# Kernel optimization log

Measured on AMD Instinct MI355X. Metric: run time of the kernel, lower is better.

## Reference

```python
import jax, jax.numpy as jnp
import numpy as np

N = 50000   # num_embs = num nodes
E = 800000  # num edges
D = 256     # feature dim
L = 4       # num layers
EPS = 1e-5


def setup_inputs() -> dict:
    key = jax.random.key(0)
    ks = jax.random.split(key, 8)
    scale = 1.0 / np.sqrt(D)
    return {
        "x": jax.random.normal(ks[0], (N, D), dtype=jnp.float32),  # ignored by forward
        "edge_index": jax.random.randint(ks[1], (2, E), 0, N, dtype=jnp.int32),
        "edge_weight": jax.random.uniform(ks[2], (E,), dtype=jnp.float32),
        "emb_weight": jax.random.normal(ks[3], (N, D), dtype=jnp.float32),
        "ln_w": jnp.ones((L, D), dtype=jnp.float32),
        "ln_b": jnp.zeros((L, D), dtype=jnp.float32),
        "conv_w": jax.random.normal(ks[4], (L, D, D), dtype=jnp.float32) * scale,
        "conv_b": jnp.zeros((L, D), dtype=jnp.float32),
        "post_w": jax.random.normal(ks[5], (D, D), dtype=jnp.float32) * scale,
        "post_b": jnp.zeros((D,), dtype=jnp.float32),
    }


def _layer_norm(h, w, b):
    mu = jnp.mean(h, axis=-1, keepdims=True)
    var = jnp.mean(jnp.square(h - mu), axis=-1, keepdims=True)
    return (h - mu) * jax.lax.rsqrt(var + EPS) * w + b


def reference(x, edge_index, edge_weight, emb_weight, ln_w, ln_b, conv_w, conv_b, post_w, post_b):
    # GCNConv semantics (PyG defaults): add self-loops (weight 1), symmetric norm.
    loop = jnp.arange(N, dtype=edge_index.dtype)
    src = jnp.concatenate([edge_index[0], loop])
    dst = jnp.concatenate([edge_index[1], loop])
    w = jnp.concatenate([edge_weight, jnp.ones((N,), edge_weight.dtype)])
    deg = jax.ops.segment_sum(w, dst, num_segments=N)
    dinv = jnp.where(deg > 0, jax.lax.rsqrt(jnp.maximum(deg, 1e-12)), 0.0)
    coef = (dinv[src] * w * dinv[dst])[:, None]  # [E+N, 1]

    h = emb_weight  # forward ignores x; cond_emb is None
    for i in range(L):
        z = _layer_norm(h, ln_w[i], ln_b[i])          # node LayerNorm
        zw = z @ conv_w[i]                             # linear transform
        agg = jax.ops.segment_sum(coef * zw[src], dst, num_segments=N)
        z = agg + conv_b[i]
        z = jax.nn.gelu(z, approximate=False)          # torch GELU is exact
        h = z + h                                      # residual (dropout=0)
    return h @ post_w + post_b
```

## Files before the change

### kernel.cpp

```cpp
#include <hip/hip_runtime.h>
#include <hip/hip_bf16.h>

#define N_NODES 50000
#define N_EDGES 800000
#define DIM     256
#define NLAYERS 4
#define EPS     1e-5f
#define SCAN_B  196
#define MASK40  ((1ULL << 40) - 1)
#define EPACK_CAP (N_EDGES + 15 * N_NODES + 32)
#define STRIDE  260
#define KSTRIDE (N_NODES * 32)

typedef __bf16 bf16x8 __attribute__((ext_vector_type(8)));
typedef float  f32x4  __attribute__((ext_vector_type(4)));
typedef float  f32x2  __attribute__((ext_vector_type(2)));
typedef unsigned short u16x8 __attribute__((ext_vector_type(8)));
typedef unsigned short u16x4 __attribute__((ext_vector_type(4)));
typedef int            i32x4 __attribute__((ext_vector_type(4)));
typedef unsigned int   u32x2 __attribute__((ext_vector_type(2)));

__device__ __forceinline__ unsigned short f2b(float f) {
    __hip_bfloat16 h = __float2bfloat16(f);
    return __builtin_bit_cast(unsigned short, h);
}
__device__ __forceinline__ float b2f(unsigned short u) {
    unsigned int v = ((unsigned int)u) << 16;
    return __builtin_bit_cast(float, v);
}
__device__ __forceinline__ float gelu_exact(float x) {
    float ax = fabsf(x) * 0.70710678118654752f;
    float t  = 1.0f / (1.0f + 0.3275911f * ax);
    float p  = t * (0.254829592f + t * (-0.284496736f +
               t * (1.421413741f + t * (-1.453152027f + t * 1.061405429f))));
    float er = 1.0f - p * __expf(-ax * ax);
    er = (x < 0.0f) ? -er : er;
    return 0.5f * x * (1.0f + er);
}
__device__ __forceinline__ unsigned int pack_fp8x4(float a, float b, float c, float d) {
    int v = 0;
    v = __builtin_amdgcn_cvt_pk_fp8_f32(a, b, v, false);
    v = __builtin_amdgcn_cvt_pk_fp8_f32(c, d, v, true);
    return (unsigned int)v;
}

__global__ __launch_bounds__(256) void hist_kernel(const int* __restrict__ dst,
                                                   const float* __restrict__ w,
                                                   unsigned long long* __restrict__ cnt64,
                                                   int* __restrict__ rank) {
    int e = blockIdx.x * 256 + threadIdx.x;
    if (e >= N_EDGES) return;
    int d = dst[e];
    unsigned long long wfix = (unsigned long long)(w[e] * 4294967296.0f);
    unsigned long long old = atomicAdd(&cnt64[d], (1ULL << 40) | wfix);
    rank[e] = (int)(old >> 40);
}

__global__ __launch_bounds__(256) void scan_a_kernel(const unsigned long long* __restrict__ cnt64,
                                                     float* __restrict__ dinv,
                                                     int* __restrict__ bsum) {
    __shared__ int l[256];
    int i = blockIdx.x * 256 + threadIdx.x;
    int pc = 0;
    if (i < N_NODES) {
        unsigned long long v = cnt64[i];
        int cnt = (int)(v >> 40);
        float sw = (float)(v & MASK40) * 2.3283064365386963e-10f;
        dinv[i] = rsqrtf(1.0f + sw);
        pc = (cnt + 15) & ~15;
    }
    l[threadIdx.x] = pc;
    __syncthreads();
    for (int o = 128; o > 0; o >>= 1) {
        if (threadIdx.x < o) l[threadIdx.x] += l[threadIdx.x + o];
        __syncthreads();
    }
    if (threadIdx.x == 0) bsum[blockIdx.x] = l[0];
}

__global__ __launch_bounds__(256) void scan_b_kernel(const int* __restrict__ bsum,
                                                     int* __restrict__ boff,
                                                     int* __restrict__ rowptr) {
    __shared__ int l[256];
    int t = threadIdx.x;
    l[t] = (t < SCAN_B) ? bsum[t] : 0;
    __syncthreads();
    if (t == 0) {
        int run = 0;
        for (int j = 0; j < SCAN_B; ++j) { int v = l[j]; l[j] = run; run += v; }
        rowptr[N_NODES] = run;
    }
    __syncthreads();
    boff[t] = l[t];
}

__global__ __launch_bounds__(256) void scan_c_kernel(const unsigned long long* __restrict__ cnt64,
                                                     const int* __restrict__ boff,
                                                     int* __restrict__ rowptr) {
    __shared__ int l[256];
    int i = blockIdx.x * 256 + threadIdx.x;
    int pc = 0;
    if (i < N_NODES) {
        int cnt = (int)(cnt64[i] >> 40);
        pc = (cnt + 15) & ~15;
    }
    l[threadIdx.x] = pc;
    __syncthreads();
    if (threadIdx.x == 0) {
        int run = 0;
        for (int j = 0; j < 256; ++j) { int v = l[j]; l[j] = run; run += v; }
    }
    __syncthreads();
    if (i < N_NODES) rowptr[i] = boff[blockIdx.x] + l[threadIdx.x];
}

__global__ __launch_bounds__(256) void fill_kernel(const int* __restrict__ src,
                                                   const int* __restrict__ dst,
                                                   const float* __restrict__ w,
                                                   const float* __restrict__ dinv,
                                                   const int* __restrict__ rowptr,
                                                   const int* __restrict__ rank,
                                                   int2* __restrict__ epack) {
    int e = blockIdx.x * 256 + threadIdx.x;
    if (e >= N_EDGES) return;
    int s = src[e], d = dst[e];
    float c = dinv[s] * w[e] * dinv[d];
    int p = rowptr[d] + rank[e];
    epack[p] = make_int2(s << 8, __float_as_int(c));
}

__global__ __launch_bounds__(256) void convw_kernel(const float* __restrict__ conv_w,
                                                    const float* __restrict__ post_w,
                                                    unsigned short* __restrict__ Wt) {
    int idx = blockIdx.x * 256 + threadIdx.x;
    if (idx >= 5 * 65536) return;
    int m  = idx >> 16;
    int r  = idx & 65535;
    int ks = r >> 13;
    int n  = (r >> 5) & 255;
    int ke = r & 31;
    int k  = ks * 32 + ke;
    float v = (m < 4) ? conv_w[m * 65536 + k * 256 + n] : post_w[k * 256 + n];
    Wt[idx] = f2b(v);
}

__global__ __launch_bounds__(256) void ln_cast_kernel(const float* __restrict__ H,
                                                      const float* __restrict__ lnw,
                                                      const float* __restrict__ lnb,
                                                      unsigned char* __restrict__ Z8,
                                                      unsigned short* __restrict__ Hbf) {
    int row = blockIdx.x * 4 + (threadIdx.x >> 6);
    int lane = threadIdx.x & 63;
    const float4 x = *(const float4*)(H + (size_t)row * DIM + lane * 4);
    float s = x.x + x.y + x.z + x.w;
    for (int o = 32; o > 0; o >>= 1) s += __shfl_xor(s, o);
    float mu = s * (1.0f / DIM);
    float d0 = x.x - mu, d1 = x.y - mu, d2 = x.z - mu, d3 = x.w - mu;
    float v = d0 * d0 + d1 * d1 + d2 * d2 + d3 * d3;
    for (int o = 32; o > 0; o >>= 1) v += __shfl_xor(v, o);
    float rs = rsqrtf(v * (1.0f / DIM) + EPS);
    const float4 ww = *(const float4*)(lnw + lane * 4);
    const float4 bb = *(const float4*)(lnb + lane * 4);
    float z0 = d0 * rs * ww.x + bb.x;
    float z1 = d1 * rs * ww.y + bb.y;
    float z2 = d2 * rs * ww.z + bb.z;
    float z3 = d3 * rs * ww.w + bb.w;
    *(unsigned int*)(Z8 + (size_t)row * DIM + lane * 4) = pack_fp8x4(z0, z1, z2, z3);
    ushort4 h4;
    h4.x = f2b(x.x); h4.y = f2b(x.y); h4.z = f2b(x.z); h4.w = f2b(x.w);
    *(ushort4*)(Hbf + (size_t)row * DIM + lane * 4) = h4;
}

__global__ __launch_bounds__(256) void agg_kernel(const unsigned char* __restrict__ Z8,
                                                  const int* __restrict__ rowptr,
                                                  const int2* __restrict__ epack,
                                                  const float* __restrict__ dinv,
                                                  unsigned short* __restrict__ AGG) {
    int node = blockIdx.x * 4 + (threadIdx.x >> 6);
    int lane = threadIdx.x & 63;
    int g = lane >> 5;
    int colB = (lane & 31) * 8;

    float di = dinv[node];
    float scg = (g == 0) ? di * di : 0.0f;
    const u32x2 zs = *(const u32x2*)(Z8 + (size_t)node * DIM + colB);
    f32x2 a0, a1, a2, a3;
    {
        f32x2 p0 = __builtin_amdgcn_cvt_pk_f32_fp8(zs[0], false);
        f32x2 p1 = __builtin_amdgcn_cvt_pk_f32_fp8(zs[0], true);
        f32x2 p2 = __builtin_amdgcn_cvt_pk_f32_fp8(zs[1], false);
        f32x2 p3 = __builtin_amdgcn_cvt_pk_f32_fp8(zs[1], true);
        a0 = scg * p0; a1 = scg * p1; a2 = scg * p2; a3 = scg * p3;
    }

    int e0 = rowptr[node], e1 = rowptr[node + 1];
    for (int e = e0; e < e1; e += 16) {
        const int2* pp = epack + e + 8 * g;
        const i32x4 q0 = *(const i32x4*)pp;
        const i32x4 q1 = *(const i32x4*)(pp + 2);
        const i32x4 q2 = *(const i32x4*)(pp + 4);
        const i32x4 q3 = *(const i32x4*)(pp + 6);
        const u32x2 v0 = *(const u32x2*)(Z8 + q0[0] + colB);
        const u32x2 v1 = *(const u32x2*)(Z8 + q0[2] + colB);
        const u32x2 v2 = *(const u32x2*)(Z8 + q1[0] + colB);
        const u32x2 v3 = *(const u32x2*)(Z8 + q1[2] + colB);
        const u32x2 v4 = *(const u32x2*)(Z8 + q2[0] + colB);
        const u32x2 v5 = *(const u32x2*)(Z8 + q2[2] + colB);
        const u32x2 v6 = *(const u32x2*)(Z8 + q3[0] + colB);
        const u32x2 v7 = *(const u32x2*)(Z8 + q3[2] + colB);
        float c0 = __int_as_float(q0[1]), c1 = __int_as_float(q0[3]);
        float c2 = __int_as_float(q1[1]), c3 = __int_as_float(q1[3]);
        float c4 = __int_as_float(q2[1]), c5 = __int_as_float(q2[3]);
        float c6 = __int_as_float(q3[1]), c7 = __int_as_float(q3[3]);
        #pragma unroll
        for (int h = 0; h < 8; ++h) {
            u32x2 vv; float cc;
            switch (h) {
                case 0: vv = v0; cc = c0; break;
                case 1: vv = v1; cc = c1; break;
                case 2: vv = v2; cc = c2; break;
                case 3: vv = v3; cc = c3; break;
                case 4: vv = v4; cc = c4; break;
                case 5: vv = v5; cc = c5; break;
                case 6: vv = v6; cc = c6; break;
                default: vv = v7; cc = c7; break;
            }
            f32x2 p0 = __builtin_amdgcn_cvt_pk_f32_fp8(vv[0], false);
            f32x2 p1 = __builtin_amdgcn_cvt_pk_f32_fp8(vv[0], true);
            f32x2 p2 = __builtin_amdgcn_cvt_pk_f32_fp8(vv[1], false);
            f32x2 p3 = __builtin_amdgcn_cvt_pk_f32_fp8(vv[1], true);
            a0 += cc * p0; a1 += cc * p1; a2 += cc * p2; a3 += cc * p3;
        }
    }
    float a[8] = {a0[0], a0[1], a1[0], a1[1], a2[0], a2[1], a3[0], a3[1]};
    #pragma unroll
    for (int j = 0; j < 8; ++j) a[j] += __shfl_xor(a[j], 32);

    if (g == 0) {
        u16x8 z;
        #pragma unroll
        for (int j = 0; j < 8; ++j) z[j] = f2b(a[j]);
        int ks  = colB >> 5;
        int off = colB & 31;
        *(u16x8*)(AGG + (size_t)ks * KSTRIDE + node * 32 + off) = z;
    }
}

__global__ __launch_bounds__(256, 4) void gemm_fused_kernel(const unsigned short* __restrict__ A,
                                                            const unsigned short* __restrict__ Bt,
                                                            const float* __restrict__ bias,
                                                            unsigned short* __restrict__ Hbf,
                                                            const float* __restrict__ lnw,
                                                            const float* __restrict__ lnb,
                                                            unsigned char* __restrict__ Z8,
                                                            int doLN) {
    __shared__ unsigned short stile[32 * STRIDE];
    int tid = threadIdx.x;
    int wave = tid >> 6;
    int lane = tid & 63;
    int q = lane >> 4;
    int c16 = lane & 15;
    int mbase = blockIdx.x * 32;
    int cbase = wave * 64;

    int aoff[2];
    #pragma unroll
    for (int nt = 0; nt < 2; ++nt) {
        int row = mbase + nt * 16 + c16;
        if (row >= N_NODES) row = N_NODES - 1;
        aoff[nt] = row * 32 + q * 8;
    }
    int woff[4];
    #pragma unroll
    for (int ct = 0; ct < 4; ++ct)
        woff[ct] = (cbase + ct * 16 + c16) * 32 + q * 8;

    f32x4 acc[2][4] = {};
    #pragma unroll
    for (int ks = 0; ks < 8; ++ks) {
        bf16x8 nf[2], wf[4];
        #pragma unroll
        for (int nt = 0; nt < 2; ++nt)
            nf[nt] = __builtin_bit_cast(bf16x8, *(const u16x8*)(A + (size_t)ks * KSTRIDE + aoff[nt]));
        #pragma unroll
        for (int ct = 0; ct < 4; ++ct)
            wf[ct] = __builtin_bit_cast(bf16x8, *(const u16x8*)(Bt + ks * 8192 + woff[ct]));
        #pragma unroll
        for (int nt = 0; nt < 2; ++nt)
            #pragma unroll
            for (int ct = 0; ct < 4; ++ct)
                acc[nt][ct] = __builtin_amdgcn_mfma_f32_16x16x32_bf16(wf[ct], nf[nt], acc[nt][ct], 0, 0, 0);
    }

    #pragma unroll
    for (int nt = 0; nt < 2; ++nt) {
        int row = nt * 16 + c16;
        #pragma unroll
        for (int ct = 0; ct < 4; ++ct) {
            int col = cbase + ct * 16 + q * 4;
            u16x4 pk;
            pk[0] = f2b(acc[nt][ct][0]);
            pk[1] = f2b(acc[nt][ct][1]);
            pk[2] = f2b(acc[nt][ct][2]);
            pk[3] = f2b(acc[nt][ct][3]);
            *(u16x4*)&stile[row * STRIDE + col] = pk;
        }
    }
    __syncthreads();

    int r  = tid >> 3;
    int cb = (tid & 7) * 32;
    int node = mbase + r;
    if (node < N_NODES) {
        float h[32];
        float psum = 0.0f, psq = 0.0f;
        #pragma unroll
        for (int i = 0; i < 4; ++i) {
            const u16x8 sv = *(const u16x8*)&stile[r * STRIDE + cb + i * 8];
            const f32x4 b0 = *(const f32x4*)(bias + cb + i * 8);
            const f32x4 b1 = *(const f32x4*)(bias + cb + i * 8 + 4);
            const u16x8 hv = *(const u16x8*)(Hbf + (size_t)node * DIM + cb + i * 8);
            #pragma unroll
            for (int j = 0; j < 8; ++j) {
                float v = b2f(sv[j]) + (j < 4 ? b0[j] : b1[j - 4]);
                float hn = gelu_exact(v) + b2f(hv[j]);
                h[i * 8 + j] = hn;
                psum += hn;
                psq += hn * hn;
            }
        }
        #pragma unroll
        for (int i = 0; i < 4; ++i) {
            u16x8 hw;
            #pragma unroll
            for (int j = 0; j < 8; ++j) hw[j] = f2b(h[i * 8 + j]);
            *(u16x8*)(Hbf + (size_t)node * DIM + cb + i * 8) = hw;
        }
        if (doLN) {
            psum += __shfl_xor(psum, 1);
            psum += __shfl_xor(psum, 2);
            psum += __shfl_xor(psum, 4);
            psq  += __shfl_xor(psq, 1);
            psq  += __shfl_xor(psq, 2);
            psq  += __shfl_xor(psq, 4);
            float mu = psum * (1.0f / DIM);
            float var = fmaxf(psq * (1.0f / DIM) - mu * mu, 0.0f);
            float rs = rsqrtf(var + EPS);
            #pragma unroll
            for (int i2 = 0; i2 < 2; ++i2) {
                int c0 = cb + i2 * 16;
                unsigned int pk[4];
                #pragma unroll
                for (int k = 0; k < 4; ++k) {
                    const f32x4 ww = *(const f32x4*)(lnw + c0 + k * 4);
                    const f32x4 lb = *(const f32x4*)(lnb + c0 + k * 4);
                    int hb = i2 * 16 + k * 4;
                    float y0 = (h[hb + 0] - mu) * rs * ww[0] + lb[0];
                    float y1 = (h[hb + 1] - mu) * rs * ww[1] + lb[1];
                    float y2 = (h[hb + 2] - mu) * rs * ww[2] + lb[2];
                    float y3 = (h[hb + 3] - mu) * rs * ww[3] + lb[3];
                    pk[k] = pack_fp8x4(y0, y1, y2, y3);
                }
                uint4 st = make_uint4(pk[0], pk[1], pk[2], pk[3]);
                *(uint4*)(Z8 + (size_t)node * DIM + c0) = st;
            }
        }
    }
}

__global__ __launch_bounds__(256, 4) void gemm_out_kernel(const unsigned short* __restrict__ A,
                                                          const unsigned short* __restrict__ Bt,
                                                          float* __restrict__ C,
                                                          const float* __restrict__ bias) {
    int tid = threadIdx.x;
    int wave = tid >> 6;
    int lane = tid & 63;
    int q = lane >> 4;
    int c16 = lane & 15;
    int mbase = blockIdx.x * 32;
    int cbase = wave * 64;

    const unsigned short* aptr[2];
    #pragma unroll
    for (int nt = 0; nt < 2; ++nt) {
        int row = mbase + nt * 16 + c16;
        if (row >= N_NODES) row = N_NODES - 1;
        aptr[nt] = A + (size_t)row * DIM + q * 8;
    }
    int woff[4];
    #pragma unroll
    for (int ct = 0; ct < 4; ++ct)
        woff[ct] = (cbase + ct * 16 + c16) * 32 + q * 8;

    f32x4 acc[2][4] = {};
    #pragma unroll
    for (int ks = 0; ks < 8; ++ks) {
        bf16x8 nf[2], wf[4];
        #pragma unroll
        for (int nt = 0; nt < 2; ++nt)
            nf[nt] = __builtin_bit_cast(bf16x8, *(const u16x8*)(aptr[nt] + ks * 32));
        #pragma unroll
        for (int ct = 0; ct < 4; ++ct)
            wf[ct] = __builtin_bit_cast(bf16x8, *(const u16x8*)(Bt + ks * 8192 + woff[ct]));
        #pragma unroll
        for (int nt = 0; nt < 2; ++nt)
            #pragma unroll
            for (int ct = 0; ct < 4; ++ct)
                acc[nt][ct] = __builtin_amdgcn_mfma_f32_16x16x32_bf16(nf[nt], wf[ct], acc[nt][ct], 0, 0, 0);
    }

    float bb[4];
    #pragma unroll
    for (int ct = 0; ct < 4; ++ct)
        bb[ct] = bias[cbase + ct * 16 + c16];
    #pragma unroll
    for (int nt = 0; nt < 2; ++nt) {
        #pragma unroll
        for (int j = 0; j < 4; ++j) {
            int node = mbase + nt * 16 + q * 4 + j;
            if (node >= N_NODES) continue;
            #pragma unroll
            for (int ct = 0; ct < 4; ++ct) {
                int chan = cbase + ct * 16 + c16;
                C[(size_t)node * DIM + chan] = acc[nt][ct][j] + bb[ct];
            }
        }
    }
}

extern "C" void kernel_launch(void* const* d_in, const int* in_sizes, int n_in,
                              void* d_out, int out_size, void* d_ws, size_t ws_size,
                              hipStream_t stream) {
    const int*   ei     = (const int*)d_in[1];
    const int*   src    = ei;
    const int*   dst    = ei + N_EDGES;
    const float* ew     = (const float*)d_in[2];
    const float* emb    = (const float*)d_in[3];
    const float* ln_w   = (const float*)d_in[4];
    const float* ln_b   = (const float*)d_in[5];
    const float* conv_w = (const float*)d_in[6];
    const float* conv_b = (const float*)d_in[7];
    const float* post_w = (const float*)d_in[8];
    const float* post_b = (const float*)d_in[9];
    float* out = (float*)d_out;

    char* w = (char*)d_ws;
    size_t off = 0;
    auto alloc = [&](size_t bytes) -> char* {
        char* p = w + off;
        off += (bytes + 255) & ~(size_t)255;
        return p;
    };
    unsigned long long* cnt64 = (unsigned long long*)alloc((size_t)N_NODES * 8);
    float* dinv   = (float*)alloc((size_t)N_NODES * 4);
    int*   rank   = (int*)alloc((size_t)N_EDGES * 4);
    int*   rowptr = (int*)alloc((size_t)(N_NODES + 1) * 4);
    int*   bsum   = (int*)alloc(256 * 4);
    int*   boff   = (int*)alloc(256 * 4);
    int2*  epack  = (int2*)alloc((size_t)EPACK_CAP * 8);
    unsigned short* Wt    = (unsigned short*)alloc((size_t)5 * 65536 * 2);
    unsigned short* AGG16 = (unsigned short*)alloc((size_t)N_NODES * DIM * 2);
    unsigned char*  Z8    = (unsigned char*)alloc((size_t)N_NODES * DIM);
    unsigned short* Hbf   = (unsigned short*)alloc((size_t)N_NODES * DIM * 2);

    hipMemsetAsync(cnt64, 0, (size_t)N_NODES * 8, stream);
    hipMemsetAsync(epack, 0, (size_t)EPACK_CAP * 8, stream);
    hist_kernel<<<N_EDGES / 256, 256, 0, stream>>>(dst, ew, cnt64, rank);
    scan_a_kernel<<<SCAN_B, 256, 0, stream>>>(cnt64, dinv, bsum);
    scan_b_kernel<<<1, 256, 0, stream>>>(bsum, boff, rowptr);
    scan_c_kernel<<<SCAN_B, 256, 0, stream>>>(cnt64, boff, rowptr);
    fill_kernel<<<N_EDGES / 256, 256, 0, stream>>>(src, dst, ew, dinv, rowptr, rank, epack);
    convw_kernel<<<(5 * 65536) / 256, 256, 0, stream>>>(conv_w, post_w, Wt);

    const int GEMM_GRID = (N_NODES + 31) / 32;
    ln_cast_kernel<<<N_NODES / 4, 256, 0, stream>>>(emb, ln_w, ln_b, Z8, Hbf);
    for (int l = 0; l < NLAYERS; ++l) {
        agg_kernel<<<N_NODES / 4, 256, 0, stream>>>(Z8, rowptr, epack, dinv, AGG16);
        int doLN = (l < NLAYERS - 1) ? 1 : 0;
        const float* nlw = doLN ? (ln_w + (l + 1) * DIM) : ln_w;
        const float* nlb = doLN ? (ln_b + (l + 1) * DIM) : ln_b;
        gemm_fused_kernel<<<GEMM_GRID, 256, 0, stream>>>(AGG16, Wt + (size_t)l * 65536,
                                                         conv_b + (size_t)l * DIM, Hbf,
                                                         nlw, nlb, Z8, doLN);
    }
    gemm_out_kernel<<<GEMM_GRID, 256, 0, stream>>>(Hbf, Wt + (size_t)4 * 65536, out, post_b);
}
```

Before: 567.0 us.

## Fuse edge aggregation into per-layer GEMM kernel via shared-memory tile

Merges the aggregation kernel into the GEMM+epilogue kernel. Each 32-node block gathers neighbour rows into an LDS tile, then runs the MFMA GEMM on it. This removes the bf16 AGG round trip through global memory and one launch per layer. Z8 is double-buffered because other blocks still read the previous layer's features. The cost is that each wave handles 8 nodes serially, which may expose gather latency and cut parallelism compared with the one-node-per-wave aggregation kernel.

```diff
diff --git a/kernel.cpp b/kernel.cpp
--- a/kernel.cpp
+++ b/kernel.cpp
@@ -9,8 +9,7 @@
 #define SCAN_B  196
 #define MASK40  ((1ULL << 40) - 1)
 #define EPACK_CAP (N_EDGES + 15 * N_NODES + 32)
-#define STRIDE  260
-#define KSTRIDE (N_NODES * 32)
+#define ASTRIDE 258
 
 typedef __bf16 bf16x8 __attribute__((ext_vector_type(8)));
 typedef float  f32x4  __attribute__((ext_vector_type(4)));
@@ -171,105 +170,99 @@
     *(ushort4*)(Hbf + (size_t)row * DIM + lane * 4) = h4;
 }
 
-__global__ __launch_bounds__(256) void agg_kernel(const unsigned char* __restrict__ Z8,
-                                                  const int* __restrict__ rowptr,
-                                                  const int2* __restrict__ epack,
-                                                  const float* __restrict__ dinv,
-                                                  unsigned short* __restrict__ AGG) {
-    int node = blockIdx.x * 4 + (threadIdx.x >> 6);
-    int lane = threadIdx.x & 63;
-    int g = lane >> 5;
-    int colB = (lane & 31) * 8;
-
-    float di = dinv[node];
-    float scg = (g == 0) ? di * di : 0.0f;
-    const u32x2 zs = *(const u32x2*)(Z8 + (size_t)node * DIM + colB);
-    f32x2 a0, a1, a2, a3;
-    {
-        f32x2 p0 = __builtin_amdgcn_cvt_pk_f32_fp8(zs[0], false);
-        f32x2 p1 = __builtin_amdgcn_cvt_pk_f32_fp8(zs[0], true);
-        f32x2 p2 = __builtin_amdgcn_cvt_pk_f32_fp8(zs[1], false);
-        f32x2 p3 = __builtin_amdgcn_cvt_pk_f32_fp8(zs[1], true);
-        a0 = scg * p0; a1 = scg * p1; a2 = scg * p2; a3 = scg * p3;
-    }
-
-    int e0 = rowptr[node], e1 = rowptr[node + 1];
-    for (int e = e0; e < e1; e += 16) {
-        const int2* pp = epack + e + 8 * g;
-        const i32x4 q0 = *(const i32x4*)pp;
-        const i32x4 q1 = *(const i32x4*)(pp + 2);
-        const i32x4 q2 = *(const i32x4*)(pp + 4);
-        const i32x4 q3 = *(const i32x4*)(pp + 6);
-        const u32x2 v0 = *(const u32x2*)(Z8 + q0[0] + colB);
-        const u32x2 v1 = *(const u32x2*)(Z8 + q0[2] + colB);
-        const u32x2 v2 = *(const u32x2*)(Z8 + q1[0] + colB);
-        const u32x2 v3 = *(const u32x2*)(Z8 + q1[2] + colB);
-        const u32x2 v4 = *(const u32x2*)(Z8 + q2[0] + colB);
-        const u32x2 v5 = *(const u32x2*)(Z8 + q2[2] + colB);
-        const u32x2 v6 = *(const u32x2*)(Z8 + q3[0] + colB);
-        const u32x2 v7 = *(const u32x2*)(Z8 + q3[2] + colB);
-        float c0 = __int_as_float(q0[1]), c1 = __int_as_float(q0[3]);
-        float c2 = __int_as_float(q1[1]), c3 = __int_as_float(q1[3]);
-        float c4 = __int_as_float(q2[1]), c5 = __int_as_float(q2[3]);
-        float c6 = __int_as_float(q3[1]), c7 = __int_as_float(q3[3]);
-        #pragma unroll
-        for (int h = 0; h < 8; ++h) {
-            u32x2 vv; float cc;
-            switch (h) {
-                case 0: vv = v0; cc = c0; break;
-                case 1: vv = v1; cc = c1; break;
-                case 2: vv = v2; cc = c2; break;
-                case 3: vv = v3; cc = c3; break;
-                case 4: vv = v4; cc = c4; break;
-                case 5: vv = v5; cc = c5; break;
-                case 6: vv = v6; cc = c6; break;
-                default: vv = v7; cc = c7; break;
-            }
-            f32x2 p0 = __builtin_amdgcn_cvt_pk_f32_fp8(vv[0], false);
-            f32x2 p1 = __builtin_amdgcn_cvt_pk_f32_fp8(vv[0], true);
-            f32x2 p2 = __builtin_amdgcn_cvt_pk_f32_fp8(vv[1], false);
-            f32x2 p3 = __builtin_amdgcn_cvt_pk_f32_fp8(vv[1], true);
-            a0 += cc * p0; a1 += cc * p1; a2 += cc * p2; a3 += cc * p3;
-        }
-    }
-    float a[8] = {a0[0], a0[1], a1[0], a1[1], a2[0], a2[1], a3[0], a3[1]};
-    #pragma unroll
-    for (int j = 0; j < 8; ++j) a[j] += __shfl_xor(a[j], 32);
-
-    if (g == 0) {
-        u16x8 z;
-        #pragma unroll
-        for (int j = 0; j < 8; ++j) z[j] = f2b(a[j]);
-        int ks  = colB >> 5;
-        int off = colB & 31;
-        *(u16x8*)(AGG + (size_t)ks * KSTRIDE + node * 32 + off) = z;
-    }
-}
-
-__global__ __launch_bounds__(256, 4) void gemm_fused_kernel(const unsigned short* __restrict__ A,
-                                                            const unsigned short* __restrict__ Bt,
-                                                            const float* __restrict__ bias,
-                                                            unsigned short* __restrict__ Hbf,
-                                                            const float* __restrict__ lnw,
-                                                            const float* __restrict__ lnb,
-                                                            unsigned char* __restrict__ Z8,
-                                                            int doLN) {
-    __shared__ unsigned short stile[32 * STRIDE];
+__global__ __launch_bounds__(256, 4) void layer_kernel(const unsigned char* __restrict__ Z8in,
+                                                       const int* __restrict__ rowptr,
+                                                       const int2* __restrict__ epack,
+                                                       const float* __restrict__ dinv,
+                                                       const unsigned short* __restrict__ Bt,
+                                                       const float* __restrict__ bias,
+                                                       unsigned short* __restrict__ Hbf,
+                                                       const float* __restrict__ lnw,
+                                                       const float* __restrict__ lnb,
+                                                       unsigned char* __restrict__ Z8out,
+                                                       int doLN) {
+    __shared__ unsigned short atile[32 * ASTRIDE];
     int tid = threadIdx.x;
     int wave = tid >> 6;
     int lane = tid & 63;
     int q = lane >> 4;
     int c16 = lane & 15;
+    int g = lane >> 5;
+    int colB = (lane & 31) * 8;
     int mbase = blockIdx.x * 32;
     int cbase = wave * 64;
 
-    int aoff[2];
-    #pragma unroll
-    for (int nt = 0; nt < 2; ++nt) {
-        int row = mbase + nt * 16 + c16;
-        if (row >= N_NODES) row = N_NODES - 1;
-        aoff[nt] = row * 32 + q * 8;
-    }
+    for (int i = 0; i < 8; ++i) {
+        int nl = wave * 8 + i;
+        int node = mbase + nl;
+        f32x2 a0 = {0.f, 0.f}, a1 = a0, a2 = a0, a3 = a0;
+        if (node < N_NODES) {
+            float di = dinv[node];
+            float scg = (g == 0) ? di * di : 0.0f;
+            const u32x2 zs = *(const u32x2*)(Z8in + (size_t)node * DIM + colB);
+            {
+                f32x2 p0 = __builtin_amdgcn_cvt_pk_f32_fp8(zs[0], false);
+                f32x2 p1 = __builtin_amdgcn_cvt_pk_f32_fp8(zs[0], true);
+                f32x2 p2 = __builtin_amdgcn_cvt_pk_f32_fp8(zs[1], false);
+                f32x2 p3 = __builtin_amdgcn_cvt_pk_f32_fp8(zs[1], true);
+                a0 = scg * p0; a1 = scg * p1; a2 = scg * p2; a3 = scg * p3;
+            }
+            int e0 = rowptr[node], e1 = rowptr[node + 1];
+            for (int e = e0; e < e1; e += 16) {
+                const int2* pp = epack + e + 8 * g;
+                const i32x4 q0 = *(const i32x4*)pp;
+                const i32x4 q1 = *(const i32x4*)(pp + 2);
+                const i32x4 q2 = *(const i32x4*)(pp + 4);
+                const i32x4 q3 = *(const i32x4*)(pp + 6);
+                const u32x2 v0 = *(const u32x2*)(Z8in + q0[0] + colB);
+                const u32x2 v1 = *(const u32x2*)(Z8in + q0[2] + colB);
+                const u32x2 v2 = *(const u32x2*)(Z8in + q1[0] + colB);
+                const u32x2 v3 = *(const u32x2*)(Z8in + q1[2] + colB);
+                const u32x2 v4 = *(const u32x2*)(Z8in + q2[0] + colB);
+                const u32x2 v5 = *(const u32x2*)(Z8in + q2[2] + colB);
+                const u32x2 v6 = *(const u32x2*)(Z8in + q3[0] + colB);
+                const u32x2 v7 = *(const u32x2*)(Z8in + q3[2] + colB);
+                float c0 = __int_as_float(q0[1]), c1 = __int_as_float(q0[3]);
+                float c2 = __int_as_float(q1[1]), c3 = __int_as_float(q1[3]);
+                float c4 = __int_as_float(q2[1]), c5 = __int_as_float(q2[3]);
+                float c6 = __int_as_float(q3[1]), c7 = __int_as_float(q3[3]);
+                #pragma unroll
+                for (int h = 0; h < 8; ++h) {
+                    u32x2 vv; float cc;
+                    switch (h) {
+                        case 0: vv = v0; cc = c0; break;
+                        case 1: vv = v1; cc = c1; break;
+                        case 2: vv = v2; cc = c2; break;
+                        case 3: vv = v3; cc = c3; break;
+                        case 4: vv = v4; cc = c4; break;
+                        case 5: vv = v5; cc = c5; break;
+                        case 6: vv = v6; cc = c6; break;
+                        default: vv = v7; cc = c7; break;
+                    }
+                    f32x2 p0 = __builtin_amdgcn_cvt_pk_f32_fp8(vv[0], false);
+                    f32x2 p1 = __builtin_amdgcn_cvt_pk_f32_fp8(vv[0], true);
+                    f32x2 p2 = __builtin_amdgcn_cvt_pk_f32_fp8(vv[1], false);
+                    f32x2 p3 = __builtin_amdgcn_cvt_pk_f32_fp8(vv[1], true);
+                    a0 += cc * p0; a1 += cc * p1; a2 += cc * p2; a3 += cc * p3;
+                }
+            }
+        }
+        float a[8] = {a0[0], a0[1], a1[0], a1[1], a2[0], a2[1], a3[0], a3[1]};
+        #pragma unroll
+        for (int j = 0; j < 8; ++j) a[j] += __shfl_xor(a[j], 32);
+        if (g == 0) {
+            u16x8 z;
+            #pragma unroll
+            for (int j = 0; j < 8; ++j) z[j] = f2b(a[j]);
+            *(u16x8*)&atile[nl * ASTRIDE + colB] = z;
+        }
+    }
+    __syncthreads();
+
+    int aoffL[2];
+    #pragma unroll
+    for (int nt = 0; nt < 2; ++nt)
+        aoffL[nt] = (nt * 16 + c16) * ASTRIDE + q * 8;
     int woff[4];
     #pragma unroll
     for (int ct = 0; ct < 4; ++ct)
@@ -281,7 +274,7 @@
         bf16x8 nf[2], wf[4];
         #pragma unroll
         for (int nt = 0; nt < 2; ++nt)
-            nf[nt] = __builtin_bit_cast(bf16x8, *(const u16x8*)(A + (size_t)ks * KSTRIDE + aoff[nt]));
+            nf[nt] = __builtin_bit_cast(bf16x8, *(const u16x8*)&atile[aoffL[nt] + ks * 32]);
         #pragma unroll
         for (int ct = 0; ct < 4; ++ct)
             wf[ct] = __builtin_bit_cast(bf16x8, *(const u16x8*)(Bt + ks * 8192 + woff[ct]));
@@ -291,6 +284,7 @@
             for (int ct = 0; ct < 4; ++ct)
                 acc[nt][ct] = __builtin_amdgcn_mfma_f32_16x16x32_bf16(wf[ct], nf[nt], acc[nt][ct], 0, 0, 0);
     }
+    __syncthreads();
 
     #pragma unroll
     for (int nt = 0; nt < 2; ++nt) {
@@ -303,7 +297,7 @@
             pk[1] = f2b(acc[nt][ct][1]);
             pk[2] = f2b(acc[nt][ct][2]);
             pk[3] = f2b(acc[nt][ct][3]);
-            *(u16x4*)&stile[row * STRIDE + col] = pk;
+            *(u16x4*)&atile[row * ASTRIDE + col] = pk;
         }
     }
     __syncthreads();
@@ -316,7 +310,7 @@
         float psum = 0.0f, psq = 0.0f;
         #pragma unroll
         for (int i = 0; i < 4; ++i) {
-            const u16x8 sv = *(const u16x8*)&stile[r * STRIDE + cb + i * 8];
+            const u16x8 sv = *(const u16x8*)&atile[r * ASTRIDE + cb + i * 8];
             const f32x4 b0 = *(const f32x4*)(bias + cb + i * 8);
             const f32x4 b1 = *(const f32x4*)(bias + cb + i * 8 + 4);
             const u16x8 hv = *(const u16x8*)(Hbf + (size_t)node * DIM + cb + i * 8);
@@ -362,7 +356,7 @@
                     pk[k] = pack_fp8x4(y0, y1, y2, y3);
                 }
                 uint4 st = make_uint4(pk[0], pk[1], pk[2], pk[3]);
-                *(uint4*)(Z8 + (size_t)node * DIM + c0) = st;
+                *(uint4*)(Z8out + (size_t)node * DIM + c0) = st;
             }
         }
     }
@@ -458,10 +452,10 @@
     int*   bsum   = (int*)alloc(256 * 4);
     int*   boff   = (int*)alloc(256 * 4);
     int2*  epack  = (int2*)alloc((size_t)EPACK_CAP * 8);
-    unsigned short* Wt    = (unsigned short*)alloc((size_t)5 * 65536 * 2);
-    unsigned short* AGG16 = (unsigned short*)alloc((size_t)N_NODES * DIM * 2);
-    unsigned char*  Z8    = (unsigned char*)alloc((size_t)N_NODES * DIM);
-    unsigned short* Hbf   = (unsigned short*)alloc((size_t)N_NODES * DIM * 2);
+    unsigned short* Wt  = (unsigned short*)alloc((size_t)5 * 65536 * 2);
+    unsigned char*  Z8a = (unsigned char*)alloc((size_t)N_NODES * DIM);
+    unsigned char*  Z8b = (unsigned char*)alloc((size_t)N_NODES * DIM);
+    unsigned short* Hbf = (unsigned short*)alloc((size_t)N_NODES * DIM * 2);
 
     hipMemsetAsync(cnt64, 0, (size_t)N_NODES * 8, stream);
     hipMemsetAsync(epack, 0, (size_t)EPACK_CAP * 8, stream);
@@ -472,16 +466,18 @@
     fill_kernel<<<N_EDGES / 256, 256, 0, stream>>>(src, dst, ew, dinv, rowptr, rank, epack);
     convw_kernel<<<(5 * 65536) / 256, 256, 0, stream>>>(conv_w, post_w, Wt);
 
-    const int GEMM_GRID = (N_NODES + 31) / 32;
-    ln_cast_kernel<<<N_NODES / 4, 256, 0, stream>>>(emb, ln_w, ln_b, Z8, Hbf);
+    const int GRID = (N_NODES + 31) / 32;
+    ln_cast_kernel<<<N_NODES / 4, 256, 0, stream>>>(emb, ln_w, ln_b, Z8a, Hbf);
     for (int l = 0; l < NLAYERS; ++l) {
-        agg_kernel<<<N_NODES / 4, 256, 0, stream>>>(Z8, rowptr, epack, dinv, AGG16);
+        const unsigned char* zin  = (l & 1) ? Z8b : Z8a;
+        unsigned char*       zout = (l & 1) ? Z8a : Z8b;
         int doLN = (l < NLAYERS - 1) ? 1 : 0;
         const float* nlw = doLN ? (ln_w + (l + 1) * DIM) : ln_w;
         const float* nlb = doLN ? (ln_b + (l + 1) * DIM) : ln_b;
-        gemm_fused_kernel<<<GEMM_GRID, 256, 0, stream>>>(AGG16, Wt + (size_t)l * 65536,
-                                                         conv_b + (size_t)l * DIM, Hbf,
-                                                         nlw, nlb, Z8, doLN);
-    }
-    gemm_out_kernel<<<GEMM_GRID, 256, 0, stream>>>(Hbf, Wt + (size_t)4 * 65536, out, post_b);
-}
+        layer_kernel<<<GRID, 256, 0, stream>>>(zin, rowptr, epack, dinv,
+                                               Wt + (size_t)l * 65536,
+                                               conv_b + (size_t)l * DIM, Hbf,
+                                               nlw, nlb, zout, doLN);
+    }
+    gemm_out_kernel<<<GRID, 256, 0, stream>>>(Hbf, Wt + (size_t)4 * 65536, out, post_b);
+}
```

Result: no change. 564.3 us (-0.5%).
